# Kernel tuning notes

Measured on AMD Instinct MI355X. Metric: run time of the kernel, lower is better.

## Reference

```python
import jax, jax.numpy as jnp
import numpy as np
import math

B, S, E, H = 4, 4096, 2048, 16
Dh = E // H  # 128


def setup_inputs() -> dict:
    key = jax.random.key(0)
    ks = jax.random.split(key, 8)
    s = 1.0 / math.sqrt(E)
    return {
        "x": jax.random.normal(ks[0], (B, S, E), dtype=jnp.float32),
        "Wz": jax.random.uniform(ks[1], (E, E), jnp.float32, -s, s),
        "bz": jax.random.uniform(ks[2], (E,), jnp.float32, -s, s),
        "Wx": jax.random.uniform(ks[3], (E, E), jnp.float32, -s, s),
        "bx": jax.random.uniform(ks[4], (E,), jnp.float32, -s, s),
        "phase": jax.random.normal(ks[5], (H, Dh), dtype=jnp.float32),
        "Wo": jax.random.uniform(ks[6], (E, E), jnp.float32, -s, s),
        "bo": jax.random.uniform(ks[7], (E,), jnp.float32, -s, s),
    }


def reference(x, Wz, bz, Wx, bx, phase, Wo, bo):
    # torch nn.Linear: y = x @ W.T + b  (W stored [out, in])
    z = x @ Wz.T + bz                     # [B,S,E]
    xs = x @ Wx.T + bx                    # [B,S,E]
    z_h = z.reshape(B, S, H, Dh)
    x_h = xs.reshape(B, S, H, Dh)
    # elementwise phase modulation of query heads
    mod = z_h * jnp.sin(phase)            # [B,S,H,Dh] * [H,Dh]
    # NOTE: heads are on axis -2 (no transpose to [B,H,S,Dh]),
    # so scores contract over Dh giving per-token HEAD-mixing: [B,S,H,H]
    scores = jnp.einsum('bshd,bsgd->bshg', mod, x_h) / math.sqrt(Dh)
    w = jax.nn.softmax(scores, axis=-1)   # softmax over head axis g
    att = jnp.einsum('bshg,bsgd->bshd', w, x_h)  # [B,S,H,Dh]
    att = att.reshape(B, S, E)
    return att @ Wo.T + bo
```

## Files before the change

kernel.cpp:

```cpp
#include <hip/hip_runtime.h>
#include <hip/hip_bf16.h>

#define TOK 16384
#define E 2048
#define DH 128

using bf16x8 = __attribute__((ext_vector_type(8))) __bf16;
using f32x4  = __attribute__((ext_vector_type(4))) float;
using u16x8  = __attribute__((ext_vector_type(8))) unsigned short;

static __device__ __forceinline__ unsigned short f2bf(float f) {
  union { float f; unsigned u; } x; x.f = f;
  unsigned r = x.u + 0x7fffu + ((x.u >> 16) & 1u);
  return (unsigned short)(r >> 16);
}

static __device__ __forceinline__ void gload_lds16(const unsigned short* g, unsigned short* l) {
  __builtin_amdgcn_global_load_lds(
      (const __attribute__((address_space(1))) void*)g,
      (__attribute__((address_space(3))) void*)l, 16, 0, 0);
}

__global__ __launch_bounds__(256) void cvt_plain(const float* __restrict__ in,
                                                 unsigned short* __restrict__ out, int n8) {
  int stride = gridDim.x * blockDim.x;
  for (int i = blockIdx.x * blockDim.x + threadIdx.x; i < n8; i += stride) {
    const float4* p = reinterpret_cast<const float4*>(in) + (size_t)i * 2;
    float4 v0 = p[0], v1 = p[1];
    u16x8 o;
    o[0] = f2bf(v0.x); o[1] = f2bf(v0.y); o[2] = f2bf(v0.z); o[3] = f2bf(v0.w);
    o[4] = f2bf(v1.x); o[5] = f2bf(v1.y); o[6] = f2bf(v1.z); o[7] = f2bf(v1.w);
    *(reinterpret_cast<u16x8*>(out) + i) = o;
  }
}

__global__ __launch_bounds__(256) void cvt_scaled(const float* __restrict__ in,
                                                  const float* __restrict__ phase,
                                                  unsigned short* __restrict__ out, int n8) {
  const float rs = 0.08838834764831845f;
  int stride = gridDim.x * blockDim.x;
  for (int i = blockIdx.x * blockDim.x + threadIdx.x; i < n8; i += stride) {
    int row = i >> 8;
    float sc = sinf(phase[row]) * rs;
    const float4* p = reinterpret_cast<const float4*>(in) + (size_t)i * 2;
    float4 v0 = p[0], v1 = p[1];
    u16x8 o;
    o[0] = f2bf(v0.x * sc); o[1] = f2bf(v0.y * sc); o[2] = f2bf(v0.z * sc); o[3] = f2bf(v0.w * sc);
    o[4] = f2bf(v1.x * sc); o[5] = f2bf(v1.y * sc); o[6] = f2bf(v1.z * sc); o[7] = f2bf(v1.w * sc);
    *(reinterpret_cast<u16x8*>(out) + i) = o;
  }
}

__global__ __launch_bounds__(256) void scale_bias2(const float* __restrict__ bz,
                                                   const float* __restrict__ bx,
                                                   const float* __restrict__ phase,
                                                   float* __restrict__ out) {
  const float rs = 0.08838834764831845f;
  int i = blockIdx.x * blockDim.x + threadIdx.x;
  if (i < E) out[i] = bz[i] * sinf(phase[i]) * rs;
  else if (i < 2 * E) out[i] = bx[i - E];
}

#define MFMA16 __builtin_amdgcn_mfma_f32_16x16x32_bf16

static __device__ __forceinline__ bf16x8 ldf32(const unsigned short* buf, int row, int slot) {
  return *reinterpret_cast<const bf16x8*>(buf + row * 32 + ((slot ^ (row & 3)) << 3));
}

template <int NCH>
static __device__ __forceinline__ void stage_tile(const unsigned short* gbase, int ld,
                                                  unsigned short* dst,
                                                  int srow, int s0, int wave) {
#pragma unroll
  for (int c = 0; c < NCH; ++c)
    gload_lds16(gbase + (size_t)(c * 64 + srow) * ld + s0 * 8,
                dst + c * 2048 + wave * 512);
}

static __device__ __forceinline__ void q8(f32x4 (&acc)[8][4], const bf16x8 (&a)[4],
                                          const bf16x8 (&b)[2], int mh, int nh) {
#pragma unroll
  for (int mi = 0; mi < 4; ++mi)
#pragma unroll
    for (int ni = 0; ni < 2; ++ni)
      acc[mh * 4 + mi][nh * 2 + ni] =
          MFMA16(a[mi], b[ni], acc[mh * 4 + mi][nh * 2 + ni], 0, 0, 0);
}

#define PH_BAR()  __builtin_amdgcn_s_barrier()
#define VMCNT(n)  asm volatile("s_waitcnt vmcnt(" #n ")" ::: "memory")
#define PRIO1()   __builtin_amdgcn_s_setprio(1)
#define PRIO0()   __builtin_amdgcn_s_setprio(0)

#define LDA32(dst, buf, base)                                            \
  _Pragma("unroll")                                                      \
  for (int mi = 0; mi < 4; ++mi)                                         \
    dst[mi] = ldf32(buf, (base) + mi * 16, grp);

#define LDB32(dst, buf, base)                                            \
  _Pragma("unroll")                                                      \
  for (int ni = 0; ni < 2; ++ni)                                         \
    dst[ni] = ldf32(buf, (base) + ni * 16, grp);

template <bool LAST>
static __device__ __forceinline__ void k_iter(
    const unsigned short* __restrict__ Ag, const unsigned short* __restrict__ Bg,
    int K_, int lda, int t,
    unsigned short* sA0, unsigned short* sA1, unsigned short* sB0, unsigned short* sB1,
    int srow, int s0, int wave, int grp, int rA, int rB, f32x4 (&acc)[8][4]) {
  const size_t k1 = (size_t)(t + 1) * 32, k2 = (size_t)(t + 2) * 32, k3 = (size_t)(t + 3) * 32;
  bf16x8 aF[4], b0[2], b1[2];

  LDA32(aF, sA0, rA);
  LDB32(b0, sB0, rB);
  LDB32(b1, sB0, rB + 32);
  stage_tile<4>(Ag + k1, lda, sA1, srow, s0, wave);
  PRIO1(); q8(acc, aF, b0, 0, 0); q8(acc, aF, b1, 0, 1); PRIO0();
  PH_BAR();

  LDA32(aF, sA0, rA + 64);
  if (!LAST) stage_tile<2>(Bg + k2, K_, sB0, srow, s0, wave);
  PRIO1(); q8(acc, aF, b1, 1, 1); q8(acc, aF, b0, 1, 0); PRIO0();
  if (!LAST) { VMCNT(2); } else { VMCNT(0); }
  PH_BAR();

  LDA32(aF, sA1, rA);
  LDB32(b0, sB1, rB);
  LDB32(b1, sB1, rB + 32);
  if (!LAST) stage_tile<4>(Ag + k2, lda, sA0, srow, s0, wave);
  PRIO1(); q8(acc, aF, b0, 0, 0); q8(acc, aF, b1, 0, 1); PRIO0();
  PH_BAR();

  LDA32(aF, sA1, rA + 64);
  if (!LAST) stage_tile<2>(Bg + k3, K_, sB1, srow, s0, wave);
  PRIO1(); q8(acc, aF, b1, 1, 1); q8(acc, aF, b0, 1, 0); PRIO0();
  if (!LAST) { VMCNT(2); }
  PH_BAR();
}

template <bool OUT_BF16>
__global__ __launch_bounds__(256, 2) void gemm256(const unsigned short* __restrict__ A,
                                                  const unsigned short* __restrict__ Bm,
                                                  const float* __restrict__ bias,
                                                  void* __restrict__ C,
                                                  int M, int N, int K_, int lda) {
  extern __shared__ unsigned short lds[];
  unsigned short* sA0 = lds;
  unsigned short* sA1 = lds + 8192;
  unsigned short* sB0 = lds + 16384;
  unsigned short* sB1 = lds + 20480;

  const int nbn = N >> 7;
  const int bid = blockIdx.x;
  const int swz = (bid & 7) * ((int)gridDim.x >> 3) + (bid >> 3);
  const int by = swz / nbn, bx = swz % nbn;
  const int tm = by << 8, tn = bx << 7;

  const int tid = threadIdx.x;
  const int wave = tid >> 6, lane = tid & 63;
  const int g16 = lane & 15, grp = lane >> 4;
  const int wm = wave >> 1, wn = wave & 1;
  const int rA = wm * 128 + g16;
  const int rB = wn * 64 + g16;
  const int srow = tid >> 2;
  const int s0 = (tid & 3) ^ (srow & 3);

  const unsigned short* Ag = A + (size_t)tm * lda;
  const unsigned short* Bg = Bm + (size_t)tn * K_;
  const size_t hA2 = (size_t)0;

  f32x4 acc[8][4];
#pragma unroll
  for (int i = 0; i < 8; ++i)
#pragma unroll
    for (int j = 0; j < 4; ++j) acc[i][j] = (f32x4){0.f, 0.f, 0.f, 0.f};

  (void)hA2;
  stage_tile<4>(Ag, lda, sA0, srow, s0, wave);
  stage_tile<2>(Bg, K_, sB0, srow, s0, wave);
  stage_tile<2>(Bg + 32, K_, sB1, srow, s0, wave);
  VMCNT(2);
  __builtin_amdgcn_s_barrier();

  const int NI = K_ >> 6;
#pragma unroll 1
  for (int i = 0; i < NI - 1; ++i)
    k_iter<false>(Ag, Bg, K_, lda, 2 * i, sA0, sA1, sB0, sB1, srow, s0, wave, grp, rA, rB, acc);
  k_iter<true>(Ag, Bg, K_, lda, 2 * (NI - 1), sA0, sA1, sB0, sB1, srow, s0, wave, grp, rA, rB, acc);

#pragma unroll
  for (int mi = 0; mi < 8; ++mi) {
#pragma unroll
    for (int ni = 0; ni < 4; ++ni) {
      const int row = tm + wm * 128 + mi * 16 + grp * 4;
      const int col = tn + wn * 64 + ni * 16 + g16;
      const float bv = bias[col];
#pragma unroll
      for (int j = 0; j < 4; ++j) {
        const float v = acc[mi][ni][j] + bv;
        if (OUT_BF16)
          ((unsigned short*)C)[(size_t)(row + j) * N + col] = f2bf(v);
        else
          ((float*)C)[(size_t)(row + j) * N + col] = v;
      }
    }
  }
}

__global__ __launch_bounds__(256) void attn_kernel(unsigned short* zc) {
  __shared__ __align__(16) unsigned short xs_lds[4][16][136];
  __shared__ float w_lds[4][16][17];

  const int wave = threadIdx.x >> 6, lane = threadIdx.x & 63;
  const int token = (blockIdx.x << 2) | wave;
  unsigned short* modp = zc + (size_t)token * (2 * E);
  const unsigned short* xsp = modp + E;
  const int g16 = lane & 15, grp = lane >> 4;

  bf16x8 a[4], b[4];
#pragma unroll
  for (int kk = 0; kk < 4; ++kk) {
    a[kk] = *reinterpret_cast<const bf16x8*>(modp + g16 * DH + kk * 32 + grp * 8);
    b[kk] = *reinterpret_cast<const bf16x8*>(xsp  + g16 * DH + kk * 32 + grp * 8);
  }
#pragma unroll
  for (int kk = 0; kk < 4; ++kk)
    *reinterpret_cast<bf16x8*>(&xs_lds[wave][g16][kk * 32 + grp * 8]) = b[kk];

  f32x4 sc = (f32x4){0.f, 0.f, 0.f, 0.f};
#pragma unroll
  for (int kk = 0; kk < 4; ++kk)
    sc = MFMA16(a[kk], b[kk], sc, 0, 0, 0);

  float w4[4];
#pragma unroll
  for (int j = 0; j < 4; ++j) {
    float s = sc[j];
    float m = s;
#pragma unroll
    for (int off = 1; off < 16; off <<= 1) m = fmaxf(m, __shfl_xor(m, off));
    float e = __expf(s - m);
    float t = e;
#pragma unroll
    for (int off = 1; off < 16; off <<= 1) t += __shfl_xor(t, off);
    w4[j] = e / t;
  }
#pragma unroll
  for (int j = 0; j < 4; ++j) w_lds[wave][grp * 4 + j][g16] = w4[j];

  __syncthreads();

  float acc[32];
#pragma unroll
  for (int i = 0; i < 32; ++i) acc[i] = 0.f;
#pragma unroll
  for (int g = 0; g < 16; ++g) {
    const float wg = w_lds[wave][g16][g];
#pragma unroll
    for (int c = 0; c < 4; ++c) {
      bf16x8 xv = *reinterpret_cast<const bf16x8*>(&xs_lds[wave][g][grp * 32 + c * 8]);
#pragma unroll
      for (int j = 0; j < 8; ++j) acc[c * 8 + j] += wg * (float)xv[j];
    }
  }

  unsigned short* op = modp + g16 * DH + grp * 32;
#pragma unroll
  for (int c = 0; c < 4; ++c) {
    u16x8 o;
#pragma unroll
    for (int j = 0; j < 8; ++j) o[j] = f2bf(acc[c * 8 + j]);
    *reinterpret_cast<u16x8*>(op + c * 8) = o;
  }
}

extern "C" void kernel_launch(void* const* d_in, const int* in_sizes, int n_in,
                              void* d_out, int out_size, void* d_ws, size_t ws_size,
                              hipStream_t stream) {
  const float* x     = (const float*)d_in[0];
  const float* Wz    = (const float*)d_in[1];
  const float* bz    = (const float*)d_in[2];
  const float* Wx    = (const float*)d_in[3];
  const float* bx    = (const float*)d_in[4];
  const float* phase = (const float*)d_in[5];
  const float* Wo    = (const float*)d_in[6];
  const float* bo    = (const float*)d_in[7];

  char* p = (char*)d_ws;
  unsigned short* x_bf  = (unsigned short*)p; p += (size_t)TOK * E * 2;
  unsigned short* C12   = (unsigned short*)p; p += (size_t)TOK * 2 * E * 2;
  unsigned short* wzx   = (unsigned short*)p; p += (size_t)2 * E * E * 2;
  unsigned short* wo_bf = (unsigned short*)p; p += (size_t)E * E * 2;
  float* bzx            = (float*)p;          p += (size_t)2 * E * 4;

  cvt_plain<<<2048, 256, 0, stream>>>(x, x_bf, TOK * E / 8);
  cvt_scaled<<<1024, 256, 0, stream>>>(Wz, phase, wzx, E * E / 8);
  cvt_plain<<<1024, 256, 0, stream>>>(Wx, wzx + (size_t)E * E, E * E / 8);
  cvt_plain<<<1024, 256, 0, stream>>>(Wo, wo_bf, E * E / 8);
  scale_bias2<<<2 * E / 256, 256, 0, stream>>>(bz, bx, phase, bzx);

  gemm256<true><<<dim3((TOK / 256) * (2 * E / 128)), 256, 49152, stream>>>(
      x_bf, wzx, bzx, C12, TOK, 2 * E, E, E);
  attn_kernel<<<TOK / 4, 256, 0, stream>>>(C12);
  gemm256<false><<<dim3((TOK / 256) * (E / 128)), 256, 49152, stream>>>(
      C12, wo_bf, bo, (float*)d_out, TOK, E, E, 2 * E);
}
```

Baseline: 530.8 us.

## Fuse prep conversions, change LDS swizzle, write attention output to compact buffer

```diff
diff --git a/kernel.cpp b/kernel.cpp
--- a/kernel.cpp
+++ b/kernel.cpp
@@ -21,50 +21,62 @@
       (__attribute__((address_space(3))) void*)l, 16, 0, 0);
 }
 
-__global__ __launch_bounds__(256) void cvt_plain(const float* __restrict__ in,
-                                                 unsigned short* __restrict__ out, int n8) {
-  int stride = gridDim.x * blockDim.x;
-  for (int i = blockIdx.x * blockDim.x + threadIdx.x; i < n8; i += stride) {
-    const float4* p = reinterpret_cast<const float4*>(in) + (size_t)i * 2;
-    float4 v0 = p[0], v1 = p[1];
-    u16x8 o;
-    o[0] = f2bf(v0.x); o[1] = f2bf(v0.y); o[2] = f2bf(v0.z); o[3] = f2bf(v0.w);
-    o[4] = f2bf(v1.x); o[5] = f2bf(v1.y); o[6] = f2bf(v1.z); o[7] = f2bf(v1.w);
-    *(reinterpret_cast<u16x8*>(out) + i) = o;
-  }
-}
-
-__global__ __launch_bounds__(256) void cvt_scaled(const float* __restrict__ in,
-                                                  const float* __restrict__ phase,
-                                                  unsigned short* __restrict__ out, int n8) {
+static __device__ __forceinline__ void cvt8(const float* __restrict__ src,
+                                            unsigned short* __restrict__ dst,
+                                            float sc) {
+  const float4* p = reinterpret_cast<const float4*>(src);
+  float4 v0 = p[0], v1 = p[1];
+  u16x8 o;
+  o[0] = f2bf(v0.x * sc); o[1] = f2bf(v0.y * sc); o[2] = f2bf(v0.z * sc); o[3] = f2bf(v0.w * sc);
+  o[4] = f2bf(v1.x * sc); o[5] = f2bf(v1.y * sc); o[6] = f2bf(v1.z * sc); o[7] = f2bf(v1.w * sc);
+  *reinterpret_cast<u16x8*>(dst) = o;
+}
+
+__global__ __launch_bounds__(256) void prep_all(const float* __restrict__ x,
+                                                const float* __restrict__ Wz,
+                                                const float* __restrict__ Wx,
+                                                const float* __restrict__ Wo,
+                                                const float* __restrict__ bz,
+                                                const float* __restrict__ bx,
+                                                const float* __restrict__ phase,
+                                                unsigned short* __restrict__ x_bf,
+                                                unsigned short* __restrict__ wzx,
+                                                unsigned short* __restrict__ wo_bf,
+                                                float* __restrict__ bzx) {
+  const int N0 = TOK * E / 8;
+  const int N1 = E * E / 8;
+  const int NB = (2 * E) / 8;
   const float rs = 0.08838834764831845f;
-  int stride = gridDim.x * blockDim.x;
-  for (int i = blockIdx.x * blockDim.x + threadIdx.x; i < n8; i += stride) {
-    int row = i >> 8;
-    float sc = sinf(phase[row]) * rs;
-    const float4* p = reinterpret_cast<const float4*>(in) + (size_t)i * 2;
-    float4 v0 = p[0], v1 = p[1];
-    u16x8 o;
-    o[0] = f2bf(v0.x * sc); o[1] = f2bf(v0.y * sc); o[2] = f2bf(v0.z * sc); o[3] = f2bf(v0.w * sc);
-    o[4] = f2bf(v1.x * sc); o[5] = f2bf(v1.y * sc); o[6] = f2bf(v1.z * sc); o[7] = f2bf(v1.w * sc);
-    *(reinterpret_cast<u16x8*>(out) + i) = o;
-  }
-}
-
-__global__ __launch_bounds__(256) void scale_bias2(const float* __restrict__ bz,
-                                                   const float* __restrict__ bx,
-                                                   const float* __restrict__ phase,
-                                                   float* __restrict__ out) {
-  const float rs = 0.08838834764831845f;
-  int i = blockIdx.x * blockDim.x + threadIdx.x;
-  if (i < E) out[i] = bz[i] * sinf(phase[i]) * rs;
-  else if (i < 2 * E) out[i] = bx[i - E];
+  const int total = N0 + 3 * N1 + NB;
+  const int stride = gridDim.x * blockDim.x;
+  for (int i = blockIdx.x * blockDim.x + threadIdx.x; i < total; i += stride) {
+    if (i < N0) {
+      cvt8(x + (size_t)i * 8, x_bf + (size_t)i * 8, 1.0f);
+    } else if (i < N0 + N1) {
+      const int j = i - N0;
+      const float sc = sinf(phase[j >> 8]) * rs;
+      cvt8(Wz + (size_t)j * 8, wzx + (size_t)j * 8, sc);
+    } else if (i < N0 + 2 * N1) {
+      const int j = i - N0 - N1;
+      cvt8(Wx + (size_t)j * 8, wzx + (size_t)E * E + (size_t)j * 8, 1.0f);
+    } else if (i < N0 + 3 * N1) {
+      const int j = i - N0 - 2 * N1;
+      cvt8(Wo + (size_t)j * 8, wo_bf + (size_t)j * 8, 1.0f);
+    } else {
+      const int j = i - N0 - 3 * N1;
+#pragma unroll
+      for (int k = 0; k < 8; ++k) {
+        const int idx = j * 8 + k;
+        bzx[idx] = (idx < E) ? bz[idx] * sinf(phase[idx]) * rs : bx[idx - E];
+      }
+    }
+  }
 }
 
 #define MFMA16 __builtin_amdgcn_mfma_f32_16x16x32_bf16
 
 static __device__ __forceinline__ bf16x8 ldf32(const unsigned short* buf, int row, int slot) {
-  return *reinterpret_cast<const bf16x8*>(buf + row * 32 + ((slot ^ (row & 3)) << 3));
+  return *reinterpret_cast<const bf16x8*>(buf + row * 32 + ((slot ^ ((row >> 1) & 3)) << 3));
 }
 
 template <int NCH>
@@ -163,11 +175,10 @@
   const int rA = wm * 128 + g16;
   const int rB = wn * 64 + g16;
   const int srow = tid >> 2;
-  const int s0 = (tid & 3) ^ (srow & 3);
+  const int s0 = (tid & 3) ^ ((srow >> 1) & 3);
 
   const unsigned short* Ag = A + (size_t)tm * lda;
   const unsigned short* Bg = Bm + (size_t)tn * K_;
-  const size_t hA2 = (size_t)0;
 
   f32x4 acc[8][4];
 #pragma unroll
@@ -175,7 +186,6 @@
 #pragma unroll
     for (int j = 0; j < 4; ++j) acc[i][j] = (f32x4){0.f, 0.f, 0.f, 0.f};
 
-  (void)hA2;
   stage_tile<4>(Ag, lda, sA0, srow, s0, wave);
   stage_tile<2>(Bg, K_, sB0, srow, s0, wave);
   stage_tile<2>(Bg + 32, K_, sB1, srow, s0, wave);
@@ -207,14 +217,15 @@
   }
 }
 
-__global__ __launch_bounds__(256) void attn_kernel(unsigned short* zc) {
-  __shared__ __align__(16) unsigned short xs_lds[4][16][136];
-  __shared__ float w_lds[4][16][17];
+__global__ __launch_bounds__(512) void attn_kernel(const unsigned short* __restrict__ zc,
+                                                   unsigned short* __restrict__ attq) {
+  __shared__ __align__(16) unsigned short xs_lds[8][16][136];
+  __shared__ float w_lds[8][16][17];
 
   const int wave = threadIdx.x >> 6, lane = threadIdx.x & 63;
-  const int token = (blockIdx.x << 2) | wave;
-  unsigned short* modp = zc + (size_t)token * (2 * E);
-  const unsigned short* xsp = modp + E;
+  const int token = (blockIdx.x << 3) | wave;
+  const unsigned short* modp = zc + (size_t)token * (2 * E);
+  const unsigned short* xsp  = modp + E;
   const int g16 = lane & 15, grp = lane >> 4;
 
   bf16x8 a[4], b[4];
@@ -264,7 +275,7 @@
     }
   }
 
-  unsigned short* op = modp + g16 * DH + grp * 32;
+  unsigned short* op = attq + (size_t)token * E + g16 * DH + grp * 32;
 #pragma unroll
   for (int c = 0; c < 4; ++c) {
     u16x8 o;
@@ -293,15 +304,11 @@
   unsigned short* wo_bf = (unsigned short*)p; p += (size_t)E * E * 2;
   float* bzx            = (float*)p;          p += (size_t)2 * E * 4;
 
-  cvt_plain<<<2048, 256, 0, stream>>>(x, x_bf, TOK * E / 8);
-  cvt_scaled<<<1024, 256, 0, stream>>>(Wz, phase, wzx, E * E / 8);
-  cvt_plain<<<1024, 256, 0, stream>>>(Wx, wzx + (size_t)E * E, E * E / 8);
-  cvt_plain<<<1024, 256, 0, stream>>>(Wo, wo_bf, E * E / 8);
-  scale_bias2<<<2 * E / 256, 256, 0, stream>>>(bz, bx, phase, bzx);
+  prep_all<<<2048, 256, 0, stream>>>(x, Wz, Wx, Wo, bz, bx, phase, x_bf, wzx, wo_bf, bzx);
 
   gemm256<true><<<dim3((TOK / 256) * (2 * E / 128)), 256, 49152, stream>>>(
       x_bf, wzx, bzx, C12, TOK, 2 * E, E, E);
-  attn_kernel<<<TOK / 4, 256, 0, stream>>>(C12);
+  attn_kernel<<<TOK / 8, 512, 0, stream>>>(C12, x_bf);
   gemm256<false><<<dim3((TOK / 256) * (E / 128)), 256, 49152, stream>>>(
-      C12, wo_bf, bo, (float*)d_out, TOK, E, E, 2 * E);
-}
+      x_bf, wo_bf, bo, (float*)d_out, TOK, E, E, E);
+}
```

Measured after the change: 505.6 us. 4.7% less time.
